# Kernel optimization log

Hardware: AMD Instinct MI355X
Metric: run time of the kernel (lower is better)

The kernel has to match this reference:

```python
import jax, jax.numpy as jnp
import numpy as np

NUM_HEADS = 8
HEAD_DIM = 16
NEG_SLOPE = 0.2


def setup_inputs() -> dict:
    key = jax.random.key(0)
    k1, k2, k3, k4, k5 = jax.random.split(key, 5)
    N, E, D_IN, D_OUT = 100000, 1600000, 128, 128
    x = jax.random.normal(k1, (N, D_IN), dtype=jnp.float32)
    edge_indices = jax.random.randint(k2, (2, E), 0, N, dtype=jnp.int64)
    W = jax.random.normal(k3, (D_OUT, D_IN), dtype=jnp.float32) * (1.0 / np.sqrt(D_IN))
    src_attn = jax.random.normal(k4, (1, NUM_HEADS, HEAD_DIM), dtype=jnp.float32) * (1.0 / np.sqrt(HEAD_DIM))
    dst_attn = jax.random.normal(k5, (1, NUM_HEADS, HEAD_DIM), dtype=jnp.float32) * (1.0 / np.sqrt(HEAD_DIM))
    return {"x": x, "edge_indices": edge_indices, "W": W, "src_attn": src_attn, "dst_attn": dst_attn}


def reference(x, edge_indices, W, src_attn, dst_attn):
    N = x.shape[0]
    # add self loops (i, i) for every node
    loops = jnp.arange(N, dtype=edge_indices.dtype)
    ei = jnp.concatenate([edge_indices, jnp.stack([loops, loops])], axis=1)  # [2, E+N]
    row, col = ei[0], ei[1]

    # linear projection + head split: [N, H, hd]
    h = (x @ W.T).reshape(N, NUM_HEADS, HEAD_DIM)

    # per-node attention logits, gathered per edge: [E', H]
    s = jnp.sum(h * src_attn, axis=-1)  # [N, H]
    d = jnp.sum(h * dst_attn, axis=-1)  # [N, H]
    e = jax.nn.leaky_relu(s[row] + d[col], negative_slope=NEG_SLOPE)  # [E', H]

    # sparse softmax over each row's neighborhood (dim=1 of the sparse matrix)
    m = jax.ops.segment_max(e, row, num_segments=N)  # [N, H]
    e = jnp.exp(e - m[row])
    z = jax.ops.segment_sum(e, row, num_segments=N)  # [N, H]
    a = e / z[row]  # [E', H]

    # per-head SpMM: out[row] += a * h[col]
    out = jax.ops.segment_sum(a[:, :, None] * h[col], row, num_segments=N)  # [N, H, hd]
    return out.reshape(N, NUM_HEADS * HEAD_DIM)
```

## Files before the change

### kernel.cpp

```cpp
#include <hip/hip_runtime.h>
#include <hip/hip_bf16.h>
#include <math.h>

#define NEG_SLOPE 0.2f

typedef __attribute__((ext_vector_type(8))) short short8v;
typedef __attribute__((ext_vector_type(4))) float f32x4;

__global__ __launch_bounds__(256) void gat_prep(
    const float* __restrict__ W, const float* __restrict__ srcA,
    const float* __restrict__ dstA, ushort* __restrict__ wbf,
    int* __restrict__ count8, int cn,
    unsigned int* __restrict__ state, int* __restrict__ ticket)
{
  int gtid = blockIdx.x * 256 + threadIdx.x;
  for (int i = gtid; i < cn; i += gridDim.x * 256)
    count8[i] = 0;
  if (gtid < 256) state[gtid] = 0;
  if (gtid == 0) *ticket = 0;

  if (gtid >= 36 * 64) return;
  int frag = gtid >> 6, lane = gtid & 63;
  int nt = frag >> 2, ks = frag & 3;
  int kbase = ks * 32 + (lane >> 4) * 8;
  ushort v[8];
  if (nt < 8) {
    int r = nt * 16 + (lane & 15);
#pragma unroll
    for (int j = 0; j < 8; ++j)
      v[j] = __bfloat16_as_ushort(__float2bfloat16(W[(size_t)r * 128 + kbase + j]));
  } else {
    int n = lane & 15;
    int hd = n & 7;
    const float* av = (n < 8) ? srcA : dstA;
#pragma unroll
    for (int j = 0; j < 8; ++j) {
      float acc = 0.f;
      int k = kbase + j;
      for (int d = 0; d < 16; ++d)
        acc += W[(size_t)(hd * 16 + d) * 128 + k] * av[hd * 16 + d];
      v[j] = __bfloat16_as_ushort(__float2bfloat16(acc));
    }
  }
  ushort* dst = wbf + ((size_t)frag * 64 + lane) * 8;
#pragma unroll
  for (int j = 0; j < 8; ++j) dst[j] = v[j];
}

__global__ __launch_bounds__(256, 2) void gat_gemm_hist(
    const float* __restrict__ x, const ushort* __restrict__ wbf,
    ushort* __restrict__ hb, float* __restrict__ s, float* __restrict__ dv,
    int N, int nchunks, int NG, int NH,
    const int* __restrict__ ei, int E, int* __restrict__ count8,
    int* __restrict__ rank, int userank)
{
  const int q = (int)blockIdx.x / 5;
  const int r5 = (int)blockIdx.x % 5;
  if (r5 < 3) {
    const int gemmId = q * 3 + r5;
    const int wave = threadIdx.x >> 6, lane = threadIdx.x & 63;
    const int lrow = lane & 15, lkg = lane >> 4;

    short8v b[36];
    const short8v* wv = (const short8v*)wbf;
#pragma unroll
    for (int f = 0; f < 36; ++f) b[f] = wv[(size_t)f * 64 + lane];

    for (int chunk = gemmId; chunk < nchunks; chunk += NG) {
      const int r0 = chunk * 64 + wave * 16;
      int arow = r0 + lrow; if (arow > N - 1) arow = N - 1;
      const float* xr = x + (size_t)arow * 128 + lkg * 8;

      f32x4 acc[9];
#pragma unroll
      for (int t = 0; t < 9; ++t) acc[t] = (f32x4){0.f, 0.f, 0.f, 0.f};

#pragma unroll
      for (int ks = 0; ks < 4; ++ks) {
        float4 x0 = *(const float4*)(xr + ks * 32);
        float4 x1 = *(const float4*)(xr + ks * 32 + 4);
        short8v a;
        a[0] = (short)__bfloat16_as_ushort(__float2bfloat16(x0.x));
        a[1] = (short)__bfloat16_as_ushort(__float2bfloat16(x0.y));
        a[2] = (short)__bfloat16_as_ushort(__float2bfloat16(x0.z));
        a[3] = (short)__bfloat16_as_ushort(__float2bfloat16(x0.w));
        a[4] = (short)__bfloat16_as_ushort(__float2bfloat16(x1.x));
        a[5] = (short)__bfloat16_as_ushort(__float2bfloat16(x1.y));
        a[6] = (short)__bfloat16_as_ushort(__float2bfloat16(x1.z));
        a[7] = (short)__bfloat16_as_ushort(__float2bfloat16(x1.w));
#pragma unroll
        for (int t = 0; t < 9; ++t)
          acc[t] = __builtin_amdgcn_mfma_f32_16x16x32_bf16(a, b[t * 4 + ks], acc[t], 0, 0, 0);
      }

      const int rbase = r0 + lkg * 4;
#pragma unroll
      for (int t = 0; t < 8; ++t) {
#pragma unroll
        for (int r = 0; r < 4; ++r) {
          int row = rbase + r;
          if (row < N)
            hb[(size_t)row * 128 + t * 16 + lrow] =
                __bfloat16_as_ushort(__float2bfloat16(acc[t][r]));
        }
      }
#pragma unroll
      for (int r = 0; r < 4; ++r) {
        int row = rbase + r;
        if (row < N) {
          if (lrow < 8) s[(size_t)row * 8 + lrow] = acc[8][r];
          else          dv[(size_t)row * 8 + (lrow - 8)] = acc[8][r];
        }
      }
    }
  } else {
    __shared__ int sh64;
    if (threadIdx.x == 0) sh64 = 1;
    __syncthreads();
    if (ei[2 * threadIdx.x + 1] != 0) sh64 = 0;
    __syncthreads();
    const int is64 = sh64;
    const int k = (int)(blockIdx.x & 7u);
    int* cnt = count8 + (size_t)k * N;

    const int histId = q * 2 + (r5 - 3);
    const int npairs = (E + 1) >> 1;
    const int pstride = NH * 256;
    for (int p = histId * 256 + threadIdx.x; p < npairs; p += pstride) {
      int r0, r1;
      const int i1ok = (2 * p + 1) < E;
      if (is64) {
        int4 rr = *(const int4*)(ei + 4 * (size_t)p);
        r0 = rr.x; r1 = rr.z;
      } else {
        int2 rr = ((const int2*)ei)[p];
        r0 = rr.x; r1 = rr.y;
      }
      int old0 = atomicAdd(&cnt[r0], 1);
      int old1 = i1ok ? atomicAdd(&cnt[r1], 1) : 0;
      if (userank) {
        if (i1ok) ((int2*)rank)[p] = make_int2(old0 | (k << 28), old1 | (k << 28));
        else      rank[2 * p] = old0 | (k << 28);
      }
    }
  }
}

template<int NPRIV>
__global__ __launch_bounds__(256) void gat_scan(
    const int* __restrict__ count8, int N, int nb,
    unsigned int* __restrict__ state, int* __restrict__ ticket,
    int* __restrict__ offsets, int* __restrict__ suboff,
    int* __restrict__ selfpos, int total, int userank)
{
  __shared__ int sbid;
  __shared__ int sm[256];
  __shared__ int sprefix;
  if (threadIdx.x == 0) sbid = atomicAdd(ticket, 1);
  __syncthreads();
  const int bid = sbid;
  const int base = bid * 1024 + threadIdx.x * 4;

  int c[4][NPRIV];
  int v[4];
  int tsum = 0;
#pragma unroll
  for (int j = 0; j < 4; ++j) {
    int idx = base + j;
    int cs = 0;
#pragma unroll
    for (int k = 0; k < NPRIV; ++k) {
      int cv = (idx < N) ? count8[(size_t)k * N + idx] : 0;
      c[j][k] = cv; cs += cv;
    }
    v[j] = (idx < N) ? cs + 1 : 0;
    tsum += v[j];
  }

  sm[threadIdx.x] = tsum;
  __syncthreads();
  int acc = tsum;
  for (int off = 1; off < 256; off <<= 1) {
    int other = (threadIdx.x >= off) ? sm[threadIdx.x - off] : 0;
    __syncthreads();
    acc += other;
    sm[threadIdx.x] = acc;
    __syncthreads();
  }
  const int blocktotal = sm[255];

  if (threadIdx.x == 0)
    __hip_atomic_store(&state[bid], (1u << 30) | (unsigned)blocktotal,
                       __ATOMIC_RELEASE, __HIP_MEMORY_SCOPE_AGENT);
  if (threadIdx.x < 64) {
    const int lane = threadIdx.x;
    int ex = 0;
    int j = bid - 1;
    while (j >= 0) {
      int idx = j - lane;
      unsigned d = (idx >= 0)
          ? __hip_atomic_load(&state[idx], __ATOMIC_ACQUIRE, __HIP_MEMORY_SCOPE_AGENT)
          : (2u << 30);
      unsigned st = d >> 30;
      unsigned long long m2 = __ballot(st == 2u);
      unsigned long long m0 = __ballot(st == 0u);
      int f2 = m2 ? ((int)__ffsll((long long)m2) - 1) : 64;
      int f0 = m0 ? ((int)__ffsll((long long)m0) - 1) : 64;
      if (f0 < f2) continue;
      int take = (lane < f2 || (lane == f2 && f2 < 64)) ? (int)(d & 0x3FFFFFFFu) : 0;
#pragma unroll
      for (int off = 1; off < 64; off <<= 1) take += __shfl_xor(take, off, 64);
      ex += take;
      if (f2 < 64) break;
      j -= 64;
    }
    if (lane == 0) {
      __hip_atomic_store(&state[bid], (2u << 30) | (unsigned)(ex + blocktotal),
                         __ATOMIC_RELEASE, __HIP_MEMORY_SCOPE_AGENT);
      sprefix = ex;
    }
  }
  __syncthreads();

  int e = sprefix + acc - tsum;
#pragma unroll
  for (int j = 0; j < 4; ++j) {
    int idx = base + j;
    if (idx < N) {
      offsets[idx] = e;
      int run = e;
#pragma unroll
      for (int k = 0; k < NPRIV; ++k) { suboff[(size_t)k * N + idx] = run; run += c[j][k]; }
      selfpos[idx] = userank ? run : e;
      e += v[j];
    }
  }
  if (bid == nb - 1 && threadIdx.x == 255) offsets[N] = total;
}

__global__ __launch_bounds__(256) void gat_scatter_rank(
    const int* __restrict__ ei, int E, int N,
    const int* __restrict__ suboff, const int* __restrict__ selfpos,
    const int* __restrict__ rank, int* __restrict__ scol)
{
  __shared__ int sh64;
  if (threadIdx.x == 0) sh64 = 1;
  __syncthreads();
  if (ei[2 * threadIdx.x + 1] != 0) sh64 = 0;
  __syncthreads();
  const int is64 = sh64;

  const int gid = blockIdx.x * 256 + threadIdx.x;
  const int stride = gridDim.x * 256;
  const int npairs = (E + 1) >> 1;
  for (int p = gid; p < npairs; p += stride) {
    int r0, r1, c0, c1;
    const int i1ok = (2 * p + 1) < E;
    if (is64) {
      int4 rr = *(const int4*)(ei + 4 * (size_t)p);
      int2 ca = *(const int2*)(ei + 2 * (size_t)E + 4 * (size_t)p);
      int2 cb = *(const int2*)(ei + 2 * (size_t)E + 4 * (size_t)p + 2);
      r0 = rr.x; r1 = rr.z; c0 = ca.x; c1 = cb.x;
    } else {
      int2 rr = ((const int2*)ei)[p];
      r0 = rr.x; r1 = rr.y;
      c0 = ei[E + 2 * p];
      c1 = i1ok ? ei[E + 2 * p + 1] : 0;
    }
    int2 pr = ((const int2*)rank)[p];
    int k0 = (int)(((unsigned)pr.x) >> 28);
    int pos0 = suboff[(size_t)k0 * N + r0] + (pr.x & 0x0FFFFFFF);
    scol[pos0] = c0;
    if (i1ok) {
      int k1 = (int)(((unsigned)pr.y) >> 28);
      int pos1 = suboff[(size_t)k1 * N + r1] + (pr.y & 0x0FFFFFFF);
      scol[pos1] = c1;
    }
  }
  for (int j = gid; j < N; j += stride)
    scol[selfpos[j]] = j;
}

__global__ __launch_bounds__(256) void gat_scatter(
    const int* __restrict__ ei, int E, int N,
    int* __restrict__ cursor, int* __restrict__ scol)
{
  __shared__ int sh64;
  if (threadIdx.x == 0) sh64 = 1;
  __syncthreads();
  if (ei[2 * threadIdx.x + 1] != 0) sh64 = 0;
  __syncthreads();
  const int is64 = sh64;

  int i = blockIdx.x * 256 + threadIdx.x;
  const int stride = gridDim.x * 256;
  const int total = E + N;
  for (; i < total; i += stride) {
    int r, c;
    if (i < E) {
      if (is64) { r = ei[2 * i]; c = ei[2 * (E + i)]; }
      else      { r = ei[i];     c = ei[E + i]; }
    } else {
      r = i - E; c = r;
    }
    int pos = atomicAdd(&cursor[r], 1);
    scol[pos] = c;
  }
}

__global__ __launch_bounds__(256) void gat_agg(
    const uint* __restrict__ hb, const float* __restrict__ s, const float* __restrict__ dv,
    const int* __restrict__ offsets, const int* __restrict__ scol,
    float* __restrict__ out, int N)
{
  int wid = (int)((blockIdx.x * 256 + threadIdx.x) >> 6);
  int lane = threadIdx.x & 63;
  if (wid >= N) return;
  const int g = lane >> 4;
  const int t = lane & 15;
  const int head = t >> 1;
  const int beg = __builtin_amdgcn_readfirstlane(offsets[wid]);
  const int end = __builtin_amdgcn_readfirstlane(offsets[wid + 1]);
  const float sl = s[wid * 8 + head];

  const char* hbp = (const char*)hb;
  const char* dvp = (const char*)dv;
  const uint hoff = (uint)t * 16u;
  const uint doff = (uint)head * 4u;

  float z = 0.f;
  float a0 = 0, a1 = 0, a2 = 0, a3 = 0, a4 = 0, a5 = 0, a6 = 0, a7 = 0;

  const int nq = (end - beg + 3) >> 2;
  const int lasti = end - 1;

  int iA = beg + g;       iA = iA < end ? iA : lasti;
  int iB = beg + 4 + g;   iB = iB < end ? iB : lasti;
  int iC = beg + 8 + g;   iC = iC < end ? iC : lasti;
  int cB = scol[iB];
  int cC = scol[iC];
  int cA = scol[iA];
  float dlA = *(const float*)(dvp + ((uint)cA * 32u + doff));
  uint4 huA = *(const uint4*)(hbp + ((uint)cA * 256u + hoff));
  float dlB = *(const float*)(dvp + ((uint)cB * 32u + doff));
  uint4 huB = *(const uint4*)(hbp + ((uint)cB * 256u + hoff));

  for (int j = 0; j < nq; ++j) {
    int iD = beg + 4 * (j + 3) + g; iD = iD < end ? iD : lasti;
    int cD = scol[iD];
    float dlC = *(const float*)(dvp + ((uint)cC * 32u + doff));
    uint4 huC = *(const uint4*)(hbp + ((uint)cC * 256u + hoff));

    float e = sl + dlA;
    e = fmaxf(e, NEG_SLOPE * e);
    float w = (beg + 4 * j + g < end) ? __expf(e) : 0.f;
    z += w;
    a0 = fmaf(w, __uint_as_float(huA.x << 16), a0);
    a1 = fmaf(w, __uint_as_float(huA.x & 0xFFFF0000u), a1);
    a2 = fmaf(w, __uint_as_float(huA.y << 16), a2);
    a3 = fmaf(w, __uint_as_float(huA.y & 0xFFFF0000u), a3);
    a4 = fmaf(w, __uint_as_float(huA.z << 16), a4);
    a5 = fmaf(w, __uint_as_float(huA.z & 0xFFFF0000u), a5);
    a6 = fmaf(w, __uint_as_float(huA.w << 16), a6);
    a7 = fmaf(w, __uint_as_float(huA.w & 0xFFFF0000u), a7);

    dlA = dlB; huA = huB;
    dlB = dlC; huB = huC;
    cC = cD;
  }

  a0 += __shfl_xor(a0, 16, 64); a0 += __shfl_xor(a0, 32, 64);
  a1 += __shfl_xor(a1, 16, 64); a1 += __shfl_xor(a1, 32, 64);
  a2 += __shfl_xor(a2, 16, 64); a2 += __shfl_xor(a2, 32, 64);
  a3 += __shfl_xor(a3, 16, 64); a3 += __shfl_xor(a3, 32, 64);
  a4 += __shfl_xor(a4, 16, 64); a4 += __shfl_xor(a4, 32, 64);
  a5 += __shfl_xor(a5, 16, 64); a5 += __shfl_xor(a5, 32, 64);
  a6 += __shfl_xor(a6, 16, 64); a6 += __shfl_xor(a6, 32, 64);
  a7 += __shfl_xor(a7, 16, 64); a7 += __shfl_xor(a7, 32, 64);
  z  += __shfl_xor(z, 16, 64);  z  += __shfl_xor(z, 32, 64);

  float inv = 1.f / z;
  if (lane < 16) {
    float4* op = (float4*)(out + (size_t)wid * 128 + t * 8);
    op[0] = make_float4(a0 * inv, a1 * inv, a2 * inv, a3 * inv);
    op[1] = make_float4(a4 * inv, a5 * inv, a6 * inv, a7 * inv);
  }
}

extern "C" void kernel_launch(void* const* d_in, const int* in_sizes, int n_in,
                              void* d_out, int out_size, void* d_ws, size_t ws_size,
                              hipStream_t stream) {
  const float* x    = (const float*)d_in[0];
  const int*   ei   = (const int*)d_in[1];
  const float* W    = (const float*)d_in[2];
  const float* srcA = (const float*)d_in[3];
  const float* dstA = (const float*)d_in[4];
  float* out = (float*)d_out;
  const int N = in_sizes[0] / 128;
  const int E = in_sizes[1] / 2;

  auto need = [&](int npriv, int userank) -> size_t {
    size_t b = (size_t)N * 128 * 2;
    b += (size_t)N * 8 * 4 * 2;
    b += 36864;
    b += (size_t)npriv * N * 4;
    b += (size_t)(N + 1) * 4;
    b += (size_t)npriv * N * 4;
    b += (size_t)N * 4;
    b += 256 * 4 + 16;
    b += (size_t)(E + N) * 4;
    if (userank) b += (size_t)(E + 1) * 4;
    return b;
  };
  int npriv = 8, userank = 1;
  if (need(8, 1) > ws_size) { npriv = 1; userank = 1; }
  if (need(1, 1) > ws_size) { npriv = 1; userank = 0; }

  ushort* hbuf = (ushort*)d_ws;
  float* s  = (float*)(hbuf + (size_t)N * 128);
  float* dv = s + (size_t)N * 8;
  ushort* wbf = (ushort*)(dv + (size_t)N * 8);
  int* count8  = (int*)((char*)wbf + 36864);
  int* offsets = count8 + (size_t)npriv * N;
  int* suboff  = offsets + (N + 1);
  int* selfpos = suboff + (size_t)npriv * N;
  unsigned int* state = (unsigned int*)(selfpos + N);
  int* ticket  = (int*)(state + 256);
  int* scol    = ticket + 4;
  int* rank    = scol + (E + N);

  const int nchunks = (N + 63) / 64;
  const int NG = 1536, NH = 1024;
  const int nb = (N + 1023) / 1024;

  gat_prep<<<2048, 256, 0, stream>>>(W, srcA, dstA, wbf, count8, npriv * N, state, ticket);
  gat_gemm_hist<<<2560, 256, 0, stream>>>(x, wbf, hbuf, s, dv, N, nchunks, NG, NH,
                                          ei, E, count8, rank, userank);
  if (npriv == 8)
    gat_scan<8><<<nb, 256, 0, stream>>>(count8, N, nb, state, ticket, offsets,
                                        suboff, selfpos, E + N, userank);
  else
    gat_scan<1><<<nb, 256, 0, stream>>>(count8, N, nb, state, ticket, offsets,
                                        suboff, selfpos, E + N, userank);
  if (userank)
    gat_scatter_rank<<<2048, 256, 0, stream>>>(ei, E, N, suboff, selfpos, rank, scol);
  else
    gat_scatter<<<2048, 256, 0, stream>>>(ei, E, N, selfpos, scol);
  gat_agg<<<(N + 3) / 4, 256, 0, stream>>>((const uint*)hbuf, s, dv, offsets, scol, out, N);
}
```

Measured before the change: 202.2 us.

## Split GEMM chunks across hist, scan and scatter kernels; handle self-loops in aggregation

The projection GEMM is split into one-chunk-per-block work and spread across three launches: the histogram kernel, the scan kernel and the scatter kernel. This lets the compute-bound GEMM overlap with the atomic-bound and latency-bound CSR-building phases instead of sharing one fused launch. Self-loop edges are no longer written into the CSR column array. The aggregation kernel now adds each node's own contribution directly, which shrinks the scan, scatter and workspace sizes. The risks are imbalance between the hard-coded chunk splits (700/250), scan blocks competing with GEMM blocks for slots, and extra launch-boundary dependencies.

```diff
diff --git a/kernel.cpp b/kernel.cpp
--- a/kernel.cpp
+++ b/kernel.cpp
@@ -47,112 +47,123 @@
   for (int j = 0; j < 8; ++j) dst[j] = v[j];
 }
 
-__global__ __launch_bounds__(256, 2) void gat_gemm_hist(
+__device__ __forceinline__ void gemm_chunk_body(
     const float* __restrict__ x, const ushort* __restrict__ wbf,
     ushort* __restrict__ hb, float* __restrict__ s, float* __restrict__ dv,
-    int N, int nchunks, int NG, int NH,
+    int N, int chunk)
+{
+  const int wave = threadIdx.x >> 6, lane = threadIdx.x & 63;
+  const int lrow = lane & 15, lkg = lane >> 4;
+
+  short8v b[36];
+  const short8v* wv = (const short8v*)wbf;
+#pragma unroll
+  for (int f = 0; f < 36; ++f) b[f] = wv[(size_t)f * 64 + lane];
+
+  const int r0 = chunk * 64 + wave * 16;
+  int arow = r0 + lrow; if (arow > N - 1) arow = N - 1;
+  const float* xr = x + (size_t)arow * 128 + lkg * 8;
+
+  f32x4 acc[9];
+#pragma unroll
+  for (int t = 0; t < 9; ++t) acc[t] = (f32x4){0.f, 0.f, 0.f, 0.f};
+
+#pragma unroll
+  for (int ks = 0; ks < 4; ++ks) {
+    float4 x0 = *(const float4*)(xr + ks * 32);
+    float4 x1 = *(const float4*)(xr + ks * 32 + 4);
+    short8v a;
+    a[0] = (short)__bfloat16_as_ushort(__float2bfloat16(x0.x));
+    a[1] = (short)__bfloat16_as_ushort(__float2bfloat16(x0.y));
+    a[2] = (short)__bfloat16_as_ushort(__float2bfloat16(x0.z));
+    a[3] = (short)__bfloat16_as_ushort(__float2bfloat16(x0.w));
+    a[4] = (short)__bfloat16_as_ushort(__float2bfloat16(x1.x));
+    a[5] = (short)__bfloat16_as_ushort(__float2bfloat16(x1.y));
+    a[6] = (short)__bfloat16_as_ushort(__float2bfloat16(x1.z));
+    a[7] = (short)__bfloat16_as_ushort(__float2bfloat16(x1.w));
+#pragma unroll
+    for (int t = 0; t < 9; ++t)
+      acc[t] = __builtin_amdgcn_mfma_f32_16x16x32_bf16(a, b[t * 4 + ks], acc[t], 0, 0, 0);
+  }
+
+  const int rbase = r0 + lkg * 4;
+#pragma unroll
+  for (int t = 0; t < 8; ++t) {
+#pragma unroll
+    for (int r = 0; r < 4; ++r) {
+      int row = rbase + r;
+      if (row < N)
+        hb[(size_t)row * 128 + t * 16 + lrow] =
+            __bfloat16_as_ushort(__float2bfloat16(acc[t][r]));
+    }
+  }
+#pragma unroll
+  for (int r = 0; r < 4; ++r) {
+    int row = rbase + r;
+    if (row < N) {
+      if (lrow < 8) s[(size_t)row * 8 + lrow] = acc[8][r];
+      else          dv[(size_t)row * 8 + (lrow - 8)] = acc[8][r];
+    }
+  }
+}
+
+__global__ __launch_bounds__(256, 2) void gat_hist_gemm(
+    const float* __restrict__ x, const ushort* __restrict__ wbf,
+    ushort* __restrict__ hb, float* __restrict__ s, float* __restrict__ dv,
+    int N, int nchunks, int c0,
     const int* __restrict__ ei, int E, int* __restrict__ count8,
-    int* __restrict__ rank, int userank)
-{
-  const int q = (int)blockIdx.x / 5;
-  const int r5 = (int)blockIdx.x % 5;
-  if (r5 < 3) {
-    const int gemmId = q * 3 + r5;
-    const int wave = threadIdx.x >> 6, lane = threadIdx.x & 63;
-    const int lrow = lane & 15, lkg = lane >> 4;
-
-    short8v b[36];
-    const short8v* wv = (const short8v*)wbf;
-#pragma unroll
-    for (int f = 0; f < 36; ++f) b[f] = wv[(size_t)f * 64 + lane];
-
-    for (int chunk = gemmId; chunk < nchunks; chunk += NG) {
-      const int r0 = chunk * 64 + wave * 16;
-      int arow = r0 + lrow; if (arow > N - 1) arow = N - 1;
-      const float* xr = x + (size_t)arow * 128 + lkg * 8;
-
-      f32x4 acc[9];
-#pragma unroll
-      for (int t = 0; t < 9; ++t) acc[t] = (f32x4){0.f, 0.f, 0.f, 0.f};
-
-#pragma unroll
-      for (int ks = 0; ks < 4; ++ks) {
-        float4 x0 = *(const float4*)(xr + ks * 32);
-        float4 x1 = *(const float4*)(xr + ks * 32 + 4);
-        short8v a;
-        a[0] = (short)__bfloat16_as_ushort(__float2bfloat16(x0.x));
-        a[1] = (short)__bfloat16_as_ushort(__float2bfloat16(x0.y));
-        a[2] = (short)__bfloat16_as_ushort(__float2bfloat16(x0.z));
-        a[3] = (short)__bfloat16_as_ushort(__float2bfloat16(x0.w));
-        a[4] = (short)__bfloat16_as_ushort(__float2bfloat16(x1.x));
-        a[5] = (short)__bfloat16_as_ushort(__float2bfloat16(x1.y));
-        a[6] = (short)__bfloat16_as_ushort(__float2bfloat16(x1.z));
-        a[7] = (short)__bfloat16_as_ushort(__float2bfloat16(x1.w));
-#pragma unroll
-        for (int t = 0; t < 9; ++t)
-          acc[t] = __builtin_amdgcn_mfma_f32_16x16x32_bf16(a, b[t * 4 + ks], acc[t], 0, 0, 0);
-      }
-
-      const int rbase = r0 + lkg * 4;
-#pragma unroll
-      for (int t = 0; t < 8; ++t) {
-#pragma unroll
-        for (int r = 0; r < 4; ++r) {
-          int row = rbase + r;
-          if (row < N)
-            hb[(size_t)row * 128 + t * 16 + lrow] =
-                __bfloat16_as_ushort(__float2bfloat16(acc[t][r]));
-        }
-      }
-#pragma unroll
-      for (int r = 0; r < 4; ++r) {
-        int row = rbase + r;
-        if (row < N) {
-          if (lrow < 8) s[(size_t)row * 8 + lrow] = acc[8][r];
-          else          dv[(size_t)row * 8 + (lrow - 8)] = acc[8][r];
-        }
-      }
-    }
-  } else {
-    __shared__ int sh64;
-    if (threadIdx.x == 0) sh64 = 1;
-    __syncthreads();
-    if (ei[2 * threadIdx.x + 1] != 0) sh64 = 0;
-    __syncthreads();
-    const int is64 = sh64;
-    const int k = (int)(blockIdx.x & 7u);
-    int* cnt = count8 + (size_t)k * N;
-
-    const int histId = q * 2 + (r5 - 3);
-    const int npairs = (E + 1) >> 1;
-    const int pstride = NH * 256;
-    for (int p = histId * 256 + threadIdx.x; p < npairs; p += pstride) {
-      int r0, r1;
-      const int i1ok = (2 * p + 1) < E;
-      if (is64) {
-        int4 rr = *(const int4*)(ei + 4 * (size_t)p);
-        r0 = rr.x; r1 = rr.z;
-      } else {
-        int2 rr = ((const int2*)ei)[p];
-        r0 = rr.x; r1 = rr.y;
-      }
-      int old0 = atomicAdd(&cnt[r0], 1);
-      int old1 = i1ok ? atomicAdd(&cnt[r1], 1) : 0;
-      if (userank) {
-        if (i1ok) ((int2*)rank)[p] = make_int2(old0 | (k << 28), old1 | (k << 28));
-        else      rank[2 * p] = old0 | (k << 28);
-      }
+    int* __restrict__ rank, int userank, int nhist)
+{
+  if ((int)blockIdx.x >= nhist) {
+    int chunk = c0 + (int)blockIdx.x - nhist;
+    if (chunk < nchunks) gemm_chunk_body(x, wbf, hb, s, dv, N, chunk);
+    return;
+  }
+  __shared__ int sh64;
+  if (threadIdx.x == 0) sh64 = 1;
+  __syncthreads();
+  if (ei[2 * threadIdx.x + 1] != 0) sh64 = 0;
+  __syncthreads();
+  const int is64 = sh64;
+  const int k = (int)(blockIdx.x & 7u);
+  int* cnt = count8 + (size_t)k * N;
+
+  const int npairs = (E + 1) >> 1;
+  const int pstride = nhist * 256;
+  for (int p = (int)blockIdx.x * 256 + threadIdx.x; p < npairs; p += pstride) {
+    int r0, r1;
+    const int i1ok = (2 * p + 1) < E;
+    if (is64) {
+      int4 rr = *(const int4*)(ei + 4 * (size_t)p);
+      r0 = rr.x; r1 = rr.z;
+    } else {
+      int2 rr = ((const int2*)ei)[p];
+      r0 = rr.x; r1 = rr.y;
+    }
+    int old0 = atomicAdd(&cnt[r0], 1);
+    int old1 = i1ok ? atomicAdd(&cnt[r1], 1) : 0;
+    if (userank) {
+      if (i1ok) ((int2*)rank)[p] = make_int2(old0 | (k << 28), old1 | (k << 28));
+      else      rank[2 * p] = old0 | (k << 28);
     }
   }
 }
 
 template<int NPRIV>
-__global__ __launch_bounds__(256) void gat_scan(
+__global__ __launch_bounds__(256, 2) void gat_scan_gemm(
     const int* __restrict__ count8, int N, int nb,
     unsigned int* __restrict__ state, int* __restrict__ ticket,
     int* __restrict__ offsets, int* __restrict__ suboff,
-    int* __restrict__ selfpos, int total, int userank)
-{
+    int* __restrict__ cursor, int total, int userank,
+    const float* __restrict__ x, const ushort* __restrict__ wbf,
+    ushort* __restrict__ hb, float* __restrict__ s, float* __restrict__ dv,
+    int nchunks, int c0)
+{
+  if ((int)blockIdx.x >= nb) {
+    int chunk = c0 + (int)blockIdx.x - nb;
+    if (chunk < nchunks) gemm_chunk_body(x, wbf, hb, s, dv, N, chunk);
+    return;
+  }
   __shared__ int sbid;
   __shared__ int sm[256];
   __shared__ int sprefix;
@@ -173,7 +184,7 @@
       int cv = (idx < N) ? count8[(size_t)k * N + idx] : 0;
       c[j][k] = cv; cs += cv;
     }
-    v[j] = (idx < N) ? cs + 1 : 0;
+    v[j] = (idx < N) ? cs : 0;
     tsum += v[j];
   }
 
@@ -231,18 +242,26 @@
       int run = e;
 #pragma unroll
       for (int k = 0; k < NPRIV; ++k) { suboff[(size_t)k * N + idx] = run; run += c[j][k]; }
-      selfpos[idx] = userank ? run : e;
+      cursor[idx] = e;
       e += v[j];
     }
   }
   if (bid == nb - 1 && threadIdx.x == 255) offsets[N] = total;
 }
 
-__global__ __launch_bounds__(256) void gat_scatter_rank(
+__global__ __launch_bounds__(256, 2) void gat_scatter_gemm(
     const int* __restrict__ ei, int E, int N,
-    const int* __restrict__ suboff, const int* __restrict__ selfpos,
-    const int* __restrict__ rank, int* __restrict__ scol)
-{
+    const int* __restrict__ suboff, const int* __restrict__ rank,
+    int* __restrict__ scol,
+    const float* __restrict__ x, const ushort* __restrict__ wbf,
+    ushort* __restrict__ hb, float* __restrict__ s, float* __restrict__ dv,
+    int nchunks, int c0, int nsc)
+{
+  if ((int)blockIdx.x >= nsc) {
+    int chunk = c0 + (int)blockIdx.x - nsc;
+    if (chunk < nchunks) gemm_chunk_body(x, wbf, hb, s, dv, N, chunk);
+    return;
+  }
   __shared__ int sh64;
   if (threadIdx.x == 0) sh64 = 1;
   __syncthreads();
@@ -250,35 +269,33 @@
   __syncthreads();
   const int is64 = sh64;
 
-  const int gid = blockIdx.x * 256 + threadIdx.x;
-  const int stride = gridDim.x * 256;
+  const int gid = (int)blockIdx.x * 256 + threadIdx.x;
+  const int stride = nsc * 256;
   const int npairs = (E + 1) >> 1;
   for (int p = gid; p < npairs; p += stride) {
-    int r0, r1, c0, c1;
+    int r0, r1, c0v, c1v;
     const int i1ok = (2 * p + 1) < E;
     if (is64) {
       int4 rr = *(const int4*)(ei + 4 * (size_t)p);
       int2 ca = *(const int2*)(ei + 2 * (size_t)E + 4 * (size_t)p);
       int2 cb = *(const int2*)(ei + 2 * (size_t)E + 4 * (size_t)p + 2);
-      r0 = rr.x; r1 = rr.z; c0 = ca.x; c1 = cb.x;
+      r0 = rr.x; r1 = rr.z; c0v = ca.x; c1v = cb.x;
     } else {
       int2 rr = ((const int2*)ei)[p];
       r0 = rr.x; r1 = rr.y;
-      c0 = ei[E + 2 * p];
-      c1 = i1ok ? ei[E + 2 * p + 1] : 0;
+      c0v = ei[E + 2 * p];
+      c1v = i1ok ? ei[E + 2 * p + 1] : 0;
     }
     int2 pr = ((const int2*)rank)[p];
     int k0 = (int)(((unsigned)pr.x) >> 28);
     int pos0 = suboff[(size_t)k0 * N + r0] + (pr.x & 0x0FFFFFFF);
-    scol[pos0] = c0;
+    scol[pos0] = c0v;
     if (i1ok) {
       int k1 = (int)(((unsigned)pr.y) >> 28);
       int pos1 = suboff[(size_t)k1 * N + r1] + (pr.y & 0x0FFFFFFF);
-      scol[pos1] = c1;
-    }
-  }
-  for (int j = gid; j < N; j += stride)
-    scol[selfpos[j]] = j;
+      scol[pos1] = c1v;
+    }
+  }
 }
 
 __global__ __launch_bounds__(256) void gat_scatter(
@@ -294,15 +311,10 @@
 
   int i = blockIdx.x * 256 + threadIdx.x;
   const int stride = gridDim.x * 256;
-  const int total = E + N;
-  for (; i < total; i += stride) {
+  for (; i < E; i += stride) {
     int r, c;
-    if (i < E) {
-      if (is64) { r = ei[2 * i]; c = ei[2 * (E + i)]; }
-      else      { r = ei[i];     c = ei[E + i]; }
-    } else {
-      r = i - E; c = r;
-    }
+    if (is64) { r = ei[2 * i]; c = ei[2 * (E + i)]; }
+    else      { r = ei[i];     c = ei[E + i]; }
     int pos = atomicAdd(&cursor[r], 1);
     scol[pos] = c;
   }
@@ -328,45 +340,59 @@
   const uint hoff = (uint)t * 16u;
   const uint doff = (uint)head * 4u;
 
-  float z = 0.f;
-  float a0 = 0, a1 = 0, a2 = 0, a3 = 0, a4 = 0, a5 = 0, a6 = 0, a7 = 0;
-
-  const int nq = (end - beg + 3) >> 2;
-  const int lasti = end - 1;
-
-  int iA = beg + g;       iA = iA < end ? iA : lasti;
-  int iB = beg + 4 + g;   iB = iB < end ? iB : lasti;
-  int iC = beg + 8 + g;   iC = iC < end ? iC : lasti;
-  int cB = scol[iB];
-  int cC = scol[iC];
-  int cA = scol[iA];
-  float dlA = *(const float*)(dvp + ((uint)cA * 32u + doff));
-  uint4 huA = *(const uint4*)(hbp + ((uint)cA * 256u + hoff));
-  float dlB = *(const float*)(dvp + ((uint)cB * 32u + doff));
-  uint4 huB = *(const uint4*)(hbp + ((uint)cB * 256u + hoff));
-
-  for (int j = 0; j < nq; ++j) {
-    int iD = beg + 4 * (j + 3) + g; iD = iD < end ? iD : lasti;
-    int cD = scol[iD];
-    float dlC = *(const float*)(dvp + ((uint)cC * 32u + doff));
-    uint4 huC = *(const uint4*)(hbp + ((uint)cC * 256u + hoff));
-
-    float e = sl + dlA;
-    e = fmaxf(e, NEG_SLOPE * e);
-    float w = (beg + 4 * j + g < end) ? __expf(e) : 0.f;
-    z += w;
-    a0 = fmaf(w, __uint_as_float(huA.x << 16), a0);
-    a1 = fmaf(w, __uint_as_float(huA.x & 0xFFFF0000u), a1);
-    a2 = fmaf(w, __uint_as_float(huA.y << 16), a2);
-    a3 = fmaf(w, __uint_as_float(huA.y & 0xFFFF0000u), a3);
-    a4 = fmaf(w, __uint_as_float(huA.z << 16), a4);
-    a5 = fmaf(w, __uint_as_float(huA.z & 0xFFFF0000u), a5);
-    a6 = fmaf(w, __uint_as_float(huA.w << 16), a6);
-    a7 = fmaf(w, __uint_as_float(huA.w & 0xFFFF0000u), a7);
-
-    dlA = dlB; huA = huB;
-    dlB = dlC; huB = huC;
-    cC = cD;
+  float dls = *(const float*)(dvp + ((uint)wid * 32u + doff));
+  uint4 hus = *(const uint4*)(hbp + ((uint)wid * 256u + hoff));
+  float es = sl + dls;
+  es = fmaxf(es, NEG_SLOPE * es);
+  float ws = (g == 0) ? __expf(es) : 0.f;
+  float z = ws;
+  float a0 = ws * __uint_as_float(hus.x << 16);
+  float a1 = ws * __uint_as_float(hus.x & 0xFFFF0000u);
+  float a2 = ws * __uint_as_float(hus.y << 16);
+  float a3 = ws * __uint_as_float(hus.y & 0xFFFF0000u);
+  float a4 = ws * __uint_as_float(hus.z << 16);
+  float a5 = ws * __uint_as_float(hus.z & 0xFFFF0000u);
+  float a6 = ws * __uint_as_float(hus.w << 16);
+  float a7 = ws * __uint_as_float(hus.w & 0xFFFF0000u);
+
+  if (end > beg) {
+    const int nq = (end - beg + 3) >> 2;
+    const int lasti = end - 1;
+
+    int iA = beg + g;       iA = iA < end ? iA : lasti;
+    int iB = beg + 4 + g;   iB = iB < end ? iB : lasti;
+    int iC = beg + 8 + g;   iC = iC < end ? iC : lasti;
+    int cB = scol[iB];
+    int cC = scol[iC];
+    int cA = scol[iA];
+    float dlA = *(const float*)(dvp + ((uint)cA * 32u + doff));
+    uint4 huA = *(const uint4*)(hbp + ((uint)cA * 256u + hoff));
+    float dlB = *(const float*)(dvp + ((uint)cB * 32u + doff));
+    uint4 huB = *(const uint4*)(hbp + ((uint)cB * 256u + hoff));
+
+    for (int j = 0; j < nq; ++j) {
+      int iD = beg + 4 * (j + 3) + g; iD = iD < end ? iD : lasti;
+      int cD = scol[iD];
+      float dlC = *(const float*)(dvp + ((uint)cC * 32u + doff));
+      uint4 huC = *(const uint4*)(hbp + ((uint)cC * 256u + hoff));
+
+      float e = sl + dlA;
+      e = fmaxf(e, NEG_SLOPE * e);
+      float w = (beg + 4 * j + g < end) ? __expf(e) : 0.f;
+      z += w;
+      a0 = fmaf(w, __uint_as_float(huA.x << 16), a0);
+      a1 = fmaf(w, __uint_as_float(huA.x & 0xFFFF0000u), a1);
+      a2 = fmaf(w, __uint_as_float(huA.y << 16), a2);
+      a3 = fmaf(w, __uint_as_float(huA.y & 0xFFFF0000u), a3);
+      a4 = fmaf(w, __uint_as_float(huA.z << 16), a4);
+      a5 = fmaf(w, __uint_as_float(huA.z & 0xFFFF0000u), a5);
+      a6 = fmaf(w, __uint_as_float(huA.w << 16), a6);
+      a7 = fmaf(w, __uint_as_float(huA.w & 0xFFFF0000u), a7);
+
+      dlA = dlB; huA = huB;
+      dlB = dlC; huB = huC;
+      cC = cD;
+    }
   }
 
   a0 += __shfl_xor(a0, 16, 64); a0 += __shfl_xor(a0, 32, 64);
@@ -408,7 +434,7 @@
     b += (size_t)npriv * N * 4;
     b += (size_t)N * 4;
     b += 256 * 4 + 16;
-    b += (size_t)(E + N) * 4;
+    b += (size_t)E * 4;
     if (userank) b += (size_t)(E + 1) * 4;
     return b;
   };
@@ -423,28 +449,37 @@
   int* count8  = (int*)((char*)wbf + 36864);
   int* offsets = count8 + (size_t)npriv * N;
   int* suboff  = offsets + (N + 1);
-  int* selfpos = suboff + (size_t)npriv * N;
-  unsigned int* state = (unsigned int*)(selfpos + N);
+  int* cursor  = suboff + (size_t)npriv * N;
+  unsigned int* state = (unsigned int*)(cursor + N);
   int* ticket  = (int*)(state + 256);
   int* scol    = ticket + 4;
-  int* rank    = scol + (E + N);
+  int* rank    = scol + E;
 
   const int nchunks = (N + 63) / 64;
-  const int NG = 1536, NH = 1024;
   const int nb = (N + 1023) / 1024;
+  const int NHIST = 1024, NSC = 1024;
+  const int C1 = nchunks < 700 ? nchunks : 700;
+  const int C2 = (C1 + 250) < nchunks ? (C1 + 250) : nchunks;
+  const int g2 = C1, g3 = C2 - C1, g4 = nchunks - C2;
 
   gat_prep<<<2048, 256, 0, stream>>>(W, srcA, dstA, wbf, count8, npriv * N, state, ticket);
-  gat_gemm_hist<<<2560, 256, 0, stream>>>(x, wbf, hbuf, s, dv, N, nchunks, NG, NH,
-                                          ei, E, count8, rank, userank);
+  gat_hist_gemm<<<NHIST + g2, 256, 0, stream>>>(x, wbf, hbuf, s, dv, N, nchunks, 0,
+                                                ei, E, count8, rank, userank, NHIST);
   if (npriv == 8)
-    gat_scan<8><<<nb, 256, 0, stream>>>(count8, N, nb, state, ticket, offsets,
-                                        suboff, selfpos, E + N, userank);
+    gat_scan_gemm<8><<<nb + g3, 256, 0, stream>>>(count8, N, nb, state, ticket, offsets,
+                                                  suboff, cursor, E, userank,
+                                                  x, wbf, hbuf, s, dv, nchunks, C1);
   else
-    gat_scan<1><<<nb, 256, 0, stream>>>(count8, N, nb, state, ticket, offsets,
-                                        suboff, selfpos, E + N, userank);
+    gat_scan_gemm<1><<<nb + g3, 256, 0, stream>>>(count8, N, nb, state, ticket, offsets,
+                                                  suboff, cursor, E, userank,
+                                                  x, wbf, hbuf, s, dv, nchunks, C1);
   if (userank)
-    gat_scatter_rank<<<2048, 256, 0, stream>>>(ei, E, N, suboff, selfpos, rank, scol);
-  else
-    gat_scatter<<<2048, 256, 0, stream>>>(ei, E, N, selfpos, scol);
+    gat_scatter_gemm<<<NSC + g4, 256, 0, stream>>>(ei, E, N, suboff, rank, scol,
+                                                   x, wbf, hbuf, s, dv, nchunks, C2, NSC);
+  else {
+    gat_scatter_gemm<<<(g4 > 0 ? g4 : 1), 256, 0, stream>>>(ei, 0, N, suboff, rank, scol,
+                                                   x, wbf, hbuf, s, dv, nchunks, C2, 0);
+    gat_scatter<<<2048, 256, 0, stream>>>(ei, E, N, cursor, scol);
+  }
   gat_agg<<<(N + 3) / 4, 256, 0, stream>>>((const uint*)hbuf, s, dv, offsets, scol, out, N);
 }
```

New measurement: 217.6 us. 7.6% more time.

## Handle self-loops implicitly in aggregation and replace prep zeroing with memsets

Applied to the files above, without the earlier changes.

Self-loop edges are no longer written into the CSR column array. The aggregation kernel now computes the self term directly from the node's own projected features before walking its neighbours, which removes N scatter writes and N gathered column reads and shrinks scol. The zeroing of the count, state and ticket buffers moves from the prep kernel to hipMemsetAsync calls, and the W-conversion kernel now launches with 9 blocks. This adds two memset launches and a per-node self-term load, and nodes with no incoming edges now take a special path.

```diff
diff --git a/kernel.cpp b/kernel.cpp
--- a/kernel.cpp
+++ b/kernel.cpp
@@ -7,18 +7,11 @@
 typedef __attribute__((ext_vector_type(8))) short short8v;
 typedef __attribute__((ext_vector_type(4))) float f32x4;
 
-__global__ __launch_bounds__(256) void gat_prep(
+__global__ __launch_bounds__(256) void gat_prep_wbf(
     const float* __restrict__ W, const float* __restrict__ srcA,
-    const float* __restrict__ dstA, ushort* __restrict__ wbf,
-    int* __restrict__ count8, int cn,
-    unsigned int* __restrict__ state, int* __restrict__ ticket)
+    const float* __restrict__ dstA, ushort* __restrict__ wbf)
 {
   int gtid = blockIdx.x * 256 + threadIdx.x;
-  for (int i = gtid; i < cn; i += gridDim.x * 256)
-    count8[i] = 0;
-  if (gtid < 256) state[gtid] = 0;
-  if (gtid == 0) *ticket = 0;
-
   if (gtid >= 36 * 64) return;
   int frag = gtid >> 6, lane = gtid & 63;
   int nt = frag >> 2, ks = frag & 3;
@@ -151,7 +144,7 @@
     const int* __restrict__ count8, int N, int nb,
     unsigned int* __restrict__ state, int* __restrict__ ticket,
     int* __restrict__ offsets, int* __restrict__ suboff,
-    int* __restrict__ selfpos, int total, int userank)
+    int* __restrict__ cursor, int total)
 {
   __shared__ int sbid;
   __shared__ int sm[256];
@@ -173,7 +166,7 @@
       int cv = (idx < N) ? count8[(size_t)k * N + idx] : 0;
       c[j][k] = cv; cs += cv;
     }
-    v[j] = (idx < N) ? cs + 1 : 0;
+    v[j] = (idx < N) ? cs : 0;
     tsum += v[j];
   }
 
@@ -231,7 +224,7 @@
       int run = e;
 #pragma unroll
       for (int k = 0; k < NPRIV; ++k) { suboff[(size_t)k * N + idx] = run; run += c[j][k]; }
-      selfpos[idx] = userank ? run : e;
+      cursor[idx] = e;
       e += v[j];
     }
   }
@@ -240,8 +233,8 @@
 
 __global__ __launch_bounds__(256) void gat_scatter_rank(
     const int* __restrict__ ei, int E, int N,
-    const int* __restrict__ suboff, const int* __restrict__ selfpos,
-    const int* __restrict__ rank, int* __restrict__ scol)
+    const int* __restrict__ suboff, const int* __restrict__ rank,
+    int* __restrict__ scol)
 {
   __shared__ int sh64;
   if (threadIdx.x == 0) sh64 = 1;
@@ -250,35 +243,33 @@
   __syncthreads();
   const int is64 = sh64;
 
-  const int gid = blockIdx.x * 256 + threadIdx.x;
+  const int gid = (int)blockIdx.x * 256 + threadIdx.x;
   const int stride = gridDim.x * 256;
   const int npairs = (E + 1) >> 1;
   for (int p = gid; p < npairs; p += stride) {
-    int r0, r1, c0, c1;
+    int r0, r1, c0v, c1v;
     const int i1ok = (2 * p + 1) < E;
     if (is64) {
       int4 rr = *(const int4*)(ei + 4 * (size_t)p);
       int2 ca = *(const int2*)(ei + 2 * (size_t)E + 4 * (size_t)p);
       int2 cb = *(const int2*)(ei + 2 * (size_t)E + 4 * (size_t)p + 2);
-      r0 = rr.x; r1 = rr.z; c0 = ca.x; c1 = cb.x;
+      r0 = rr.x; r1 = rr.z; c0v = ca.x; c1v = cb.x;
     } else {
       int2 rr = ((const int2*)ei)[p];
       r0 = rr.x; r1 = rr.y;
-      c0 = ei[E + 2 * p];
-      c1 = i1ok ? ei[E + 2 * p + 1] : 0;
+      c0v = ei[E + 2 * p];
+      c1v = i1ok ? ei[E + 2 * p + 1] : 0;
     }
     int2 pr = ((const int2*)rank)[p];
     int k0 = (int)(((unsigned)pr.x) >> 28);
     int pos0 = suboff[(size_t)k0 * N + r0] + (pr.x & 0x0FFFFFFF);
-    scol[pos0] = c0;
+    scol[pos0] = c0v;
     if (i1ok) {
       int k1 = (int)(((unsigned)pr.y) >> 28);
       int pos1 = suboff[(size_t)k1 * N + r1] + (pr.y & 0x0FFFFFFF);
-      scol[pos1] = c1;
-    }
-  }
-  for (int j = gid; j < N; j += stride)
-    scol[selfpos[j]] = j;
+      scol[pos1] = c1v;
+    }
+  }
 }
 
 __global__ __launch_bounds__(256) void gat_scatter(
@@ -294,15 +285,10 @@
 
   int i = blockIdx.x * 256 + threadIdx.x;
   const int stride = gridDim.x * 256;
-  const int total = E + N;
-  for (; i < total; i += stride) {
+  for (; i < E; i += stride) {
     int r, c;
-    if (i < E) {
-      if (is64) { r = ei[2 * i]; c = ei[2 * (E + i)]; }
-      else      { r = ei[i];     c = ei[E + i]; }
-    } else {
-      r = i - E; c = r;
-    }
+    if (is64) { r = ei[2 * i]; c = ei[2 * (E + i)]; }
+    else      { r = ei[i];     c = ei[E + i]; }
     int pos = atomicAdd(&cursor[r], 1);
     scol[pos] = c;
   }
@@ -328,45 +314,59 @@
   const uint hoff = (uint)t * 16u;
   const uint doff = (uint)head * 4u;
 
-  float z = 0.f;
-  float a0 = 0, a1 = 0, a2 = 0, a3 = 0, a4 = 0, a5 = 0, a6 = 0, a7 = 0;
-
-  const int nq = (end - beg + 3) >> 2;
-  const int lasti = end - 1;
-
-  int iA = beg + g;       iA = iA < end ? iA : lasti;
-  int iB = beg + 4 + g;   iB = iB < end ? iB : lasti;
-  int iC = beg + 8 + g;   iC = iC < end ? iC : lasti;
-  int cB = scol[iB];
-  int cC = scol[iC];
-  int cA = scol[iA];
-  float dlA = *(const float*)(dvp + ((uint)cA * 32u + doff));
-  uint4 huA = *(const uint4*)(hbp + ((uint)cA * 256u + hoff));
-  float dlB = *(const float*)(dvp + ((uint)cB * 32u + doff));
-  uint4 huB = *(const uint4*)(hbp + ((uint)cB * 256u + hoff));
-
-  for (int j = 0; j < nq; ++j) {
-    int iD = beg + 4 * (j + 3) + g; iD = iD < end ? iD : lasti;
-    int cD = scol[iD];
-    float dlC = *(const float*)(dvp + ((uint)cC * 32u + doff));
-    uint4 huC = *(const uint4*)(hbp + ((uint)cC * 256u + hoff));
-
-    float e = sl + dlA;
-    e = fmaxf(e, NEG_SLOPE * e);
-    float w = (beg + 4 * j + g < end) ? __expf(e) : 0.f;
-    z += w;
-    a0 = fmaf(w, __uint_as_float(huA.x << 16), a0);
-    a1 = fmaf(w, __uint_as_float(huA.x & 0xFFFF0000u), a1);
-    a2 = fmaf(w, __uint_as_float(huA.y << 16), a2);
-    a3 = fmaf(w, __uint_as_float(huA.y & 0xFFFF0000u), a3);
-    a4 = fmaf(w, __uint_as_float(huA.z << 16), a4);
-    a5 = fmaf(w, __uint_as_float(huA.z & 0xFFFF0000u), a5);
-    a6 = fmaf(w, __uint_as_float(huA.w << 16), a6);
-    a7 = fmaf(w, __uint_as_float(huA.w & 0xFFFF0000u), a7);
-
-    dlA = dlB; huA = huB;
-    dlB = dlC; huB = huC;
-    cC = cD;
+  float dls = *(const float*)(dvp + ((uint)wid * 32u + doff));
+  uint4 hus = *(const uint4*)(hbp + ((uint)wid * 256u + hoff));
+  float es = sl + dls;
+  es = fmaxf(es, NEG_SLOPE * es);
+  float ws = (g == 0) ? __expf(es) : 0.f;
+  float z = ws;
+  float a0 = ws * __uint_as_float(hus.x << 16);
+  float a1 = ws * __uint_as_float(hus.x & 0xFFFF0000u);
+  float a2 = ws * __uint_as_float(hus.y << 16);
+  float a3 = ws * __uint_as_float(hus.y & 0xFFFF0000u);
+  float a4 = ws * __uint_as_float(hus.z << 16);
+  float a5 = ws * __uint_as_float(hus.z & 0xFFFF0000u);
+  float a6 = ws * __uint_as_float(hus.w << 16);
+  float a7 = ws * __uint_as_float(hus.w & 0xFFFF0000u);
+
+  if (end > beg) {
+    const int nq = (end - beg + 3) >> 2;
+    const int lasti = end - 1;
+
+    int iA = beg + g;       iA = iA < end ? iA : lasti;
+    int iB = beg + 4 + g;   iB = iB < end ? iB : lasti;
+    int iC = beg + 8 + g;   iC = iC < end ? iC : lasti;
+    int cB = scol[iB];
+    int cC = scol[iC];
+    int cA = scol[iA];
+    float dlA = *(const float*)(dvp + ((uint)cA * 32u + doff));
+    uint4 huA = *(const uint4*)(hbp + ((uint)cA * 256u + hoff));
+    float dlB = *(const float*)(dvp + ((uint)cB * 32u + doff));
+    uint4 huB = *(const uint4*)(hbp + ((uint)cB * 256u + hoff));
+
+    for (int j = 0; j < nq; ++j) {
+      int iD = beg + 4 * (j + 3) + g; iD = iD < end ? iD : lasti;
+      int cD = scol[iD];
+      float dlC = *(const float*)(dvp + ((uint)cC * 32u + doff));
+      uint4 huC = *(const uint4*)(hbp + ((uint)cC * 256u + hoff));
+
+      float e = sl + dlA;
+      e = fmaxf(e, NEG_SLOPE * e);
+      float w = (beg + 4 * j + g < end) ? __expf(e) : 0.f;
+      z += w;
+      a0 = fmaf(w, __uint_as_float(huA.x << 16), a0);
+      a1 = fmaf(w, __uint_as_float(huA.x & 0xFFFF0000u), a1);
+      a2 = fmaf(w, __uint_as_float(huA.y << 16), a2);
+      a3 = fmaf(w, __uint_as_float(huA.y & 0xFFFF0000u), a3);
+      a4 = fmaf(w, __uint_as_float(huA.z << 16), a4);
+      a5 = fmaf(w, __uint_as_float(huA.z & 0xFFFF0000u), a5);
+      a6 = fmaf(w, __uint_as_float(huA.w << 16), a6);
+      a7 = fmaf(w, __uint_as_float(huA.w & 0xFFFF0000u), a7);
+
+      dlA = dlB; huA = huB;
+      dlB = dlC; huB = huC;
+      cC = cD;
+    }
   }
 
   a0 += __shfl_xor(a0, 16, 64); a0 += __shfl_xor(a0, 32, 64);
@@ -408,7 +408,7 @@
     b += (size_t)npriv * N * 4;
     b += (size_t)N * 4;
     b += 256 * 4 + 16;
-    b += (size_t)(E + N) * 4;
+    b += (size_t)E * 4;
     if (userank) b += (size_t)(E + 1) * 4;
     return b;
   };
@@ -423,28 +423,30 @@
   int* count8  = (int*)((char*)wbf + 36864);
   int* offsets = count8 + (size_t)npriv * N;
   int* suboff  = offsets + (N + 1);
-  int* selfpos = suboff + (size_t)npriv * N;
-  unsigned int* state = (unsigned int*)(selfpos + N);
+  int* cursor  = suboff + (size_t)npriv * N;
+  unsigned int* state = (unsigned int*)(cursor + N);
   int* ticket  = (int*)(state + 256);
   int* scol    = ticket + 4;
-  int* rank    = scol + (E + N);
+  int* rank    = scol + E;
 
   const int nchunks = (N + 63) / 64;
+  const int nb = (N + 1023) / 1024;
   const int NG = 1536, NH = 1024;
-  const int nb = (N + 1023) / 1024;
-
-  gat_prep<<<2048, 256, 0, stream>>>(W, srcA, dstA, wbf, count8, npriv * N, state, ticket);
+
+  (void)hipMemsetAsync(count8, 0, (size_t)npriv * N * sizeof(int), stream);
+  (void)hipMemsetAsync(state, 0, 256 * sizeof(int) + 16, stream);
+  gat_prep_wbf<<<9, 256, 0, stream>>>(W, srcA, dstA, wbf);
   gat_gemm_hist<<<2560, 256, 0, stream>>>(x, wbf, hbuf, s, dv, N, nchunks, NG, NH,
                                           ei, E, count8, rank, userank);
   if (npriv == 8)
     gat_scan<8><<<nb, 256, 0, stream>>>(count8, N, nb, state, ticket, offsets,
-                                        suboff, selfpos, E + N, userank);
+                                        suboff, cursor, E);
   else
     gat_scan<1><<<nb, 256, 0, stream>>>(count8, N, nb, state, ticket, offsets,
-                                        suboff, selfpos, E + N, userank);
+                                        suboff, cursor, E);
   if (userank)
-    gat_scatter_rank<<<2048, 256, 0, stream>>>(ei, E, N, suboff, selfpos, rank, scol);
+    gat_scatter_rank<<<2048, 256, 0, stream>>>(ei, E, N, suboff, rank, scol);
   else
-    gat_scatter<<<2048, 256, 0, stream>>>(ei, E, N, selfpos, scol);
+    gat_scatter<<<2048, 256, 0, stream>>>(ei, E, N, cursor, scol);
   gat_agg<<<(N + 3) / 4, 256, 0, stream>>>((const uint*)hbuf, s, dv, offsets, scol, out, N);
 }
```

After: 211.8 us. 4.7% more time.
